# Performance work log

Measured on AMD Instinct MI355X. Metric: run time of the kernel, lower is better.

## Reference

```python
import jax, jax.numpy as jnp
import numpy as np

N = 50000          # nodes
E = 600000         # edges
D = 128            # g_dim = h1_dim = h2_dim
R = 8              # 2 * n_speakers**2, n_speakers=2
B = 10             # num_bases


def setup_inputs() -> dict:
    key = jax.random.key(0)
    ks = jax.random.split(key, 10)
    s = 1.0 / np.sqrt(D)
    return {
        "node_features": jax.random.normal(ks[0], (N, D), jnp.float32),
        "edge_index": jax.random.randint(ks[1], (2, E), 0, N, jnp.int64),
        "edge_type": jax.random.randint(ks[2], (E,), 0, R, jnp.int64),
        # RGCNConv params (basis decomposition)
        "basis": jax.random.normal(ks[3], (B, D, D), jnp.float32) * s,
        "comp": jax.random.normal(ks[4], (R, B), jnp.float32) * (1.0 / np.sqrt(B)),
        "root": jax.random.normal(ks[5], (D, D), jnp.float32) * s,
        "bias1": jnp.zeros((D,), jnp.float32),
        # GraphConv params
        "w_rel": jax.random.normal(ks[6], (D, D), jnp.float32) * s,
        "b_rel": jnp.zeros((D,), jnp.float32),
        "w_root": jax.random.normal(ks[7], (D, D), jnp.float32) * s,
    }


def reference(node_features, edge_index, edge_type, basis, comp, root, bias1, w_rel, b_rel, w_root):
    x = node_features
    n = x.shape[0]
    r = comp.shape[0]
    src, dst = edge_index[0], edge_index[1]

    # ---- RGCNConv (basis decomposition, per-relation mean aggregation) ----
    # project through bases once: [N, B, D]
    xb = jnp.einsum('ni,bio->nbo', x, basis)
    # per-edge message: combine bases with relation coefficients  [E, D]
    msg = jnp.einsum('eb,ebo->eo', comp[edge_type], xb[src])
    # per-(dst, relation) mean normalization
    seg = dst * r + edge_type                       # [E]
    cnt = jax.ops.segment_sum(jnp.ones((msg.shape[0],), x.dtype), seg, num_segments=n * r)
    norm = 1.0 / jnp.maximum(cnt[seg], 1.0)         # [E]
    agg = jax.ops.segment_sum(msg * norm[:, None], dst, num_segments=n)  # [N, D]
    h1 = agg + x @ root + bias1

    # ---- GraphConv (add aggregation of neighbors + root transform) ----
    nbr = jax.ops.segment_sum(h1[src], dst, num_segments=n)  # [N, D]
    out = nbr @ w_rel.T + b_rel + h1 @ w_root.T
    return out
```

## Files before the change

kernel.cpp:

```cpp
#include <hip/hip_runtime.h>
#include <stdint.h>

#define N_NODES 50000
#define E_EDGES 600000
#define D 128
#define R_REL 8
#define B_BASES 10
#define RN (R_REL * N_NODES)

typedef __attribute__((ext_vector_type(8))) short bf16x8;
typedef __attribute__((ext_vector_type(4))) float f32x4;

__device__ __forceinline__ short f2b(float f) {
    uint32_t u = __float_as_uint(f);
    u += 0x7fff + ((u >> 16) & 1);
    return (short)(u >> 16);
}
__device__ __forceinline__ float b2f(uint16_t u) {
    return __uint_as_float((uint32_t)u << 16);
}

__global__ __launch_bounds__(256) void k_front(const float* __restrict__ x,
                                               unsigned short* __restrict__ xb,
                                               const int* __restrict__ dst,
                                               const int* __restrict__ et,
                                               int* __restrict__ cntr,
                                               const float* __restrict__ basis,
                                               const float* __restrict__ comp,
                                               const float* __restrict__ root,
                                               const float* __restrict__ wrel,
                                               const float* __restrict__ wroot,
                                               short* __restrict__ wt,
                                               short* __restrict__ wrel_b,
                                               short* __restrict__ wroot_b) {
    const int XB_N = N_NODES * D / 8;
    int tid = blockIdx.x * 256 + threadIdx.x;
    if (tid < XB_N) {
        const float4* s = (const float4*)x + (size_t)tid * 2;
        float4 v0 = s[0], v1 = s[1];
        union { uint4 u; unsigned short h[8]; } pk;
        pk.h[0] = (unsigned short)f2b(v0.x); pk.h[1] = (unsigned short)f2b(v0.y);
        pk.h[2] = (unsigned short)f2b(v0.z); pk.h[3] = (unsigned short)f2b(v0.w);
        pk.h[4] = (unsigned short)f2b(v1.x); pk.h[5] = (unsigned short)f2b(v1.y);
        pk.h[6] = (unsigned short)f2b(v1.z); pk.h[7] = (unsigned short)f2b(v1.w);
        ((uint4*)xb)[tid] = pk.u;
    } else if (tid < XB_N + E_EDGES) {
        int e = tid - XB_N;
        atomicAdd(&cntr[dst[e] * R_REL + et[e]], 1);
    } else {
        int t2 = tid - XB_N - E_EDGES;
        if (t2 < 9 * D * D) {
            int s = t2 >> 14;
            int rem = t2 & 16383;
            int j = rem >> 7, i = rem & 127;
            float v;
            if (s < 8) {
                v = 0.f;
#pragma unroll
                for (int b = 0; b < B_BASES; b++)
                    v += comp[s * B_BASES + b] * basis[b * D * D + i * D + j];
            } else {
                v = root[i * D + j];
            }
            wt[t2] = f2b(v);
        } else {
            int t3 = t2 - 9 * D * D;
            if (t3 < D * D) {
                wrel_b[t3]  = f2b(wrel[t3]);
                wroot_b[t3] = f2b(wroot[t3]);
            }
        }
    }
}

__device__ __forceinline__ int wave_scan_incl(int v) {
    int lane = threadIdx.x & 63;
#pragma unroll
    for (int off = 1; off < 64; off <<= 1) {
        int n = __shfl_up(v, off, 64);
        if (lane >= off) v += n;
    }
    return v;
}

__global__ __launch_bounds__(1024) void k_scan_a(const int* __restrict__ in,
                                                 int* __restrict__ out,
                                                 int* __restrict__ bsum, int n) {
    __shared__ int wsum[16];
    int t = threadIdx.x, lane = t & 63, wid = t >> 6;
    int g = blockIdx.x * 1024 + t;
    int v = (g < n) ? in[g] : 0;
    int isc = wave_scan_incl(v);
    if (lane == 63) wsum[wid] = isc;
    __syncthreads();
    if (wid == 0) {
        int wv = (lane < 16) ? wsum[lane] : 0;
        int wsc = wave_scan_incl(wv);
        if (lane < 16) wsum[lane] = wsc - wv;
    }
    __syncthreads();
    if (g < n) out[g] = wsum[wid] + isc - v;
    if (t == 1023 && bsum) bsum[blockIdx.x] = wsum[15] + isc;
}

__global__ __launch_bounds__(1024) void k_scan_c(int* __restrict__ out,
                                                 const int* __restrict__ bsum, int n) {
    int g = blockIdx.x * 1024 + threadIdx.x;
    if (g < n) out[g] += bsum[blockIdx.x];
}

__global__ __launch_bounds__(256) void k_bucket(const int* __restrict__ src,
                                                const int* __restrict__ dst,
                                                const int* __restrict__ et,
                                                int* __restrict__ seg_off,
                                                int* __restrict__ es1) {
    int e = blockIdx.x * 256 + threadIdx.x;
    if (e >= E_EDGES) return;
    int key = dst[e] * R_REL + et[e];
    int pos = atomicAdd(&seg_off[key], 1);
    es1[pos] = src[e];
}

__global__ __launch_bounds__(256) void k_aggmean(const unsigned short* __restrict__ xb,
                                                 const int* __restrict__ es1,
                                                 const int* __restrict__ seg_off,
                                                 unsigned short* __restrict__ mx) {
    int t = threadIdx.x;
    int sw = t >> 4, l = t & 15;
    int k = blockIdx.x * 16 + sw;
    if (k >= RN) return;
    int start = (k == 0) ? 0 : seg_off[k - 1];
    int end = seg_off[k];
    float ax[8];
#pragma unroll
    for (int q = 0; q < 8; q++) ax[q] = 0.f;
    size_t loff = (size_t)l * 8;
    int pos = start;
    for (; pos + 2 <= end; pos += 2) {
        int s0 = es1[pos], s1 = es1[pos + 1];
        uint4 v0 = *(const uint4*)(xb + (size_t)s0 * D + loff);
        uint4 v1 = *(const uint4*)(xb + (size_t)s1 * D + loff);
        const uint32_t* w0 = (const uint32_t*)&v0;
        const uint32_t* w1 = (const uint32_t*)&v1;
#pragma unroll
        for (int q = 0; q < 4; q++) {
            ax[q * 2]     += b2f((uint16_t)w0[q]) + b2f((uint16_t)w1[q]);
            ax[q * 2 + 1] += b2f((uint16_t)(w0[q] >> 16)) + b2f((uint16_t)(w1[q] >> 16));
        }
    }
    if (pos < end) {
        int s0 = es1[pos];
        uint4 v0 = *(const uint4*)(xb + (size_t)s0 * D + loff);
        const uint32_t* w0 = (const uint32_t*)&v0;
#pragma unroll
        for (int q = 0; q < 4; q++) {
            ax[q * 2]     += b2f((uint16_t)w0[q]);
            ax[q * 2 + 1] += b2f((uint16_t)(w0[q] >> 16));
        }
    }
    float nm = (end > start) ? 1.f / (float)(end - start) : 0.f;
    union { uint4 u; unsigned short h[8]; } pk;
#pragma unroll
    for (int q = 0; q < 8; q++) pk.h[q] = (unsigned short)f2b(ax[q] * nm);
    *(uint4*)(mx + (size_t)k * D + loff) = pk.u;
}

__global__ __launch_bounds__(256) void k_h1_gemm(const unsigned short* __restrict__ mx,
                                                 const unsigned short* __restrict__ xb,
                                                 const short* __restrict__ wt,
                                                 const float* __restrict__ bias1,
                                                 unsigned short* __restrict__ h1b) {
    __shared__ short xs[64 * 128];
    __shared__ short ws[128 * 128];
    int base = blockIdx.x * 64;
    int t = threadIdx.x;
    int wave = t >> 6, lane = t & 63, quad = lane >> 4, l16 = lane & 15;
    f32x4 acc[8];
#pragma unroll
    for (int jt = 0; jt < 8; jt++) acc[jt] = (f32x4){0.f, 0.f, 0.f, 0.f};

    for (int s = 0; s < 9; s++) {
        __syncthreads();
        const uint4* wsrc = (const uint4*)(wt + (size_t)s * D * D);
        for (int idx = t; idx < 2048; idx += 256) {
            int j = idx >> 4, c = idx & 15;
            *(uint4*)&ws[j * 128 + ((c ^ (j & 15)) << 3)] = wsrc[idx];
        }
        for (int idx = t; idx < 1024; idx += 256) {
            int row = idx >> 4, c = idx & 15;
            int node = base + row;
            uint4 v = make_uint4(0, 0, 0, 0);
            if (node < N_NODES) {
                if (s < 8) v = ((const uint4*)(mx + ((size_t)node * 8 + s) * D))[c];
                else       v = ((const uint4*)(xb + (size_t)node * D))[c];
            }
            *(uint4*)&xs[row * 128 + ((c ^ (row & 15)) << 3)] = v;
        }
        __syncthreads();
#pragma unroll
        for (int kc = 0; kc < 4; kc++) {
            int c0 = kc * 4 + quad;
            bf16x8 a = *(const bf16x8*)&xs[(wave * 16 + l16) * 128 + ((c0 ^ l16) << 3)];
#pragma unroll
            for (int jt = 0; jt < 8; jt++) {
                bf16x8 b = *(const bf16x8*)&ws[(jt * 16 + l16) * 128 + ((c0 ^ l16) << 3)];
                acc[jt] = __builtin_amdgcn_mfma_f32_16x16x32_bf16(a, b, acc[jt], 0, 0, 0);
            }
        }
    }

#pragma unroll
    for (int reg = 0; reg < 4; reg++) {
        int node = base + wave * 16 + quad * 4 + reg;
        if (node >= N_NODES) continue;
#pragma unroll
        for (int jt = 0; jt < 8; jt++) {
            int col = jt * 16 + l16;
            float v = acc[jt][reg] + bias1[col];
            h1b[(size_t)node * D + col] = (unsigned short)f2b(v);
        }
    }
}

__global__ __launch_bounds__(256) void k_agg_nbr(const unsigned short* __restrict__ h1b,
                                                 const int* __restrict__ es1,
                                                 const int* __restrict__ seg_off,
                                                 unsigned short* __restrict__ nbr) {
    int t = threadIdx.x;
    int wave = t >> 6, lane = t & 63, sub = lane >> 4, l = lane & 15;
    int d = blockIdx.x * 16 + wave * 4 + sub;
    if (d >= N_NODES) return;
    int start = (d == 0) ? 0 : seg_off[d * R_REL - 1];
    int end = seg_off[d * R_REL + 7];
    float acc[8];
#pragma unroll
    for (int j = 0; j < 8; j++) acc[j] = 0.f;
    size_t loff = (size_t)l * 8;

    int pos = start;
    for (; pos + 4 <= end; pos += 4) {
        int i0 = es1[pos], i1 = es1[pos + 1], i2 = es1[pos + 2], i3 = es1[pos + 3];
        uint4 v0 = *(const uint4*)(h1b + (size_t)i0 * D + loff);
        uint4 v1 = *(const uint4*)(h1b + (size_t)i1 * D + loff);
        uint4 v2 = *(const uint4*)(h1b + (size_t)i2 * D + loff);
        uint4 v3 = *(const uint4*)(h1b + (size_t)i3 * D + loff);
        const uint32_t* w0 = (const uint32_t*)&v0;
        const uint32_t* w1 = (const uint32_t*)&v1;
        const uint32_t* w2 = (const uint32_t*)&v2;
        const uint32_t* w3 = (const uint32_t*)&v3;
#pragma unroll
        for (int q = 0; q < 4; q++) {
            acc[q * 2]     += b2f((uint16_t)w0[q]) + b2f((uint16_t)w1[q]) +
                              b2f((uint16_t)w2[q]) + b2f((uint16_t)w3[q]);
            acc[q * 2 + 1] += b2f((uint16_t)(w0[q] >> 16)) + b2f((uint16_t)(w1[q] >> 16)) +
                              b2f((uint16_t)(w2[q] >> 16)) + b2f((uint16_t)(w3[q] >> 16));
        }
    }
    for (; pos < end; pos++) {
        int i0 = es1[pos];
        uint4 v0 = *(const uint4*)(h1b + (size_t)i0 * D + loff);
        const uint32_t* w0 = (const uint32_t*)&v0;
#pragma unroll
        for (int q = 0; q < 4; q++) {
            acc[q * 2]     += b2f((uint16_t)w0[q]);
            acc[q * 2 + 1] += b2f((uint16_t)(w0[q] >> 16));
        }
    }

    union { uint4 u; unsigned short h[8]; } pk;
#pragma unroll
    for (int j = 0; j < 8; j++) pk.h[j] = (unsigned short)f2b(acc[j]);
    *(uint4*)(nbr + (size_t)d * D + loff) = pk.u;
}

__global__ __launch_bounds__(256) void k_out2(const unsigned short* __restrict__ h1b,
                                              const unsigned short* __restrict__ nbr,
                                              const short* __restrict__ wroot_b,
                                              const short* __restrict__ wrel_b,
                                              const float* __restrict__ brel,
                                              float* __restrict__ out) {
    __shared__ short xs1[64 * 128];
    __shared__ short xs2[64 * 128];
    __shared__ short ws1[128 * 128];
    __shared__ short ws2[128 * 128];
    int base = blockIdx.x * 64;
    int t = threadIdx.x;
    const uint4* w1 = (const uint4*)wroot_b;
    const uint4* w2 = (const uint4*)wrel_b;
    for (int idx = t; idx < 2048; idx += 256) {
        int j = idx >> 4, c = idx & 15;
        int sw = j * 128 + ((c ^ (j & 15)) << 3);
        *(uint4*)&ws1[sw] = w1[idx];
        *(uint4*)&ws2[sw] = w2[idx];
    }
    for (int idx = t; idx < 1024; idx += 256) {
        int row = idx >> 4, c = idx & 15;
        int node = base + row;
        uint4 v1 = make_uint4(0, 0, 0, 0), v2 = make_uint4(0, 0, 0, 0);
        if (node < N_NODES) {
            v1 = ((const uint4*)(h1b + (size_t)node * D))[c];
            v2 = ((const uint4*)(nbr + (size_t)node * D))[c];
        }
        int sw = row * 128 + ((c ^ (row & 15)) << 3);
        *(uint4*)&xs1[sw] = v1;
        *(uint4*)&xs2[sw] = v2;
    }
    __syncthreads();

    int wave = t >> 6, lane = t & 63, quad = lane >> 4, l16 = lane & 15;
    f32x4 acc[8];
#pragma unroll
    for (int jt = 0; jt < 8; jt++) acc[jt] = (f32x4){0.f, 0.f, 0.f, 0.f};
#pragma unroll
    for (int kc = 0; kc < 4; kc++) {
        int c0 = kc * 4 + quad;
        int arow = (wave * 16 + l16) * 128 + ((c0 ^ l16) << 3);
        bf16x8 a1 = *(const bf16x8*)&xs1[arow];
        bf16x8 a2 = *(const bf16x8*)&xs2[arow];
#pragma unroll
        for (int jt = 0; jt < 8; jt++) {
            int brow = (jt * 16 + l16) * 128 + ((c0 ^ l16) << 3);
            bf16x8 b1 = *(const bf16x8*)&ws1[brow];
            bf16x8 b2 = *(const bf16x8*)&ws2[brow];
            acc[jt] = __builtin_amdgcn_mfma_f32_16x16x32_bf16(a1, b1, acc[jt], 0, 0, 0);
            acc[jt] = __builtin_amdgcn_mfma_f32_16x16x32_bf16(a2, b2, acc[jt], 0, 0, 0);
        }
    }
#pragma unroll
    for (int reg = 0; reg < 4; reg++) {
        int node = base + wave * 16 + quad * 4 + reg;
        if (node >= N_NODES) continue;
#pragma unroll
        for (int jt = 0; jt < 8; jt++) {
            int col = jt * 16 + l16;
            out[(size_t)node * D + col] = acc[jt][reg] + brel[col];
        }
    }
}

extern "C" void kernel_launch(void* const* d_in, const int* in_sizes, int n_in,
                              void* d_out, int out_size, void* d_ws, size_t ws_size,
                              hipStream_t stream) {
    const float* x     = (const float*)d_in[0];
    const int*   ei    = (const int*)d_in[1];
    const int*   et    = (const int*)d_in[2];
    const float* basis = (const float*)d_in[3];
    const float* comp  = (const float*)d_in[4];
    const float* root  = (const float*)d_in[5];
    const float* bias1 = (const float*)d_in[6];
    const float* wrel  = (const float*)d_in[7];
    const float* brel  = (const float*)d_in[8];
    const float* wroot = (const float*)d_in[9];
    float* out = (float*)d_out;
    const int* src = ei;
    const int* dst = ei + E_EDGES;

    char* p = (char*)d_ws;
    auto alloc = [&](size_t bytes) { char* q = p; p += (bytes + 255) & ~(size_t)255; return q; };
    short* wt      = (short*)alloc((size_t)9 * D * D * sizeof(short));
    short* wrel_b  = (short*)alloc(D * D * sizeof(short));
    short* wroot_b = (short*)alloc(D * D * sizeof(short));
    int*   cntr    = (int*)alloc((size_t)RN * sizeof(int));
    int*   seg_off = (int*)alloc((size_t)RN * sizeof(int));
    int*   es1     = (int*)alloc((size_t)(E_EDGES + 16) * sizeof(int));
    int*   bsum    = (int*)alloc(1024 * sizeof(int));
    unsigned short* xb  = (unsigned short*)alloc((size_t)N_NODES * D * sizeof(unsigned short));
    unsigned short* mx  = (unsigned short*)alloc((size_t)RN * D * sizeof(unsigned short));
    unsigned short* h1b = (unsigned short*)alloc((size_t)N_NODES * D * sizeof(unsigned short));
    unsigned short* nbr = xb;

    hipMemsetAsync(cntr, 0, (size_t)RN * sizeof(int), stream);

    const int XB_N = N_NODES * D / 8;
    int nfront = (XB_N + E_EDGES + 9 * D * D + D * D + 255) / 256;
    k_front<<<nfront, 256, 0, stream>>>(x, xb, dst, et, cntr,
                                        basis, comp, root, wrel, wroot,
                                        wt, wrel_b, wroot_b);

    int nscan = (RN + 1023) / 1024;
    k_scan_a<<<nscan, 1024, 0, stream>>>(cntr, seg_off, bsum, RN);
    k_scan_a<<<1, 1024, 0, stream>>>(bsum, bsum, nullptr, nscan);
    k_scan_c<<<nscan, 1024, 0, stream>>>(seg_off, bsum, RN);

    k_bucket<<<(E_EDGES + 255) / 256, 256, 0, stream>>>(src, dst, et, seg_off, es1);

    k_aggmean<<<RN / 16, 256, 0, stream>>>(xb, es1, seg_off, mx);

    int nb = (N_NODES + 63) / 64;
    int na = (N_NODES + 15) / 16;
    k_h1_gemm<<<nb, 256, 0, stream>>>(mx, xb, wt, bias1, h1b);
    k_agg_nbr<<<na, 256, 0, stream>>>(h1b, es1, seg_off, nbr);
    k_out2<<<nb, 256, 0, stream>>>(h1b, nbr, wroot_b, wrel_b, brel, out);
}
```

Measured before the change: 311.6 us.

## Load GEMM operands directly from global memory instead of staging through LDS

```diff
diff --git a/kernel.cpp b/kernel.cpp
--- a/kernel.cpp
+++ b/kernel.cpp
@@ -170,40 +170,27 @@
                                                  const short* __restrict__ wt,
                                                  const float* __restrict__ bias1,
                                                  unsigned short* __restrict__ h1b) {
-    __shared__ short xs[64 * 128];
-    __shared__ short ws[128 * 128];
-    int base = blockIdx.x * 64;
     int t = threadIdx.x;
     int wave = t >> 6, lane = t & 63, quad = lane >> 4, l16 = lane & 15;
+    int arow_idx = blockIdx.x * 64 + wave * 16 + l16;
+    bool valid = arow_idx < N_NODES;
+    int nodeC = valid ? arow_idx : N_NODES - 1;
     f32x4 acc[8];
 #pragma unroll
     for (int jt = 0; jt < 8; jt++) acc[jt] = (f32x4){0.f, 0.f, 0.f, 0.f};
 
     for (int s = 0; s < 9; s++) {
-        __syncthreads();
-        const uint4* wsrc = (const uint4*)(wt + (size_t)s * D * D);
-        for (int idx = t; idx < 2048; idx += 256) {
-            int j = idx >> 4, c = idx & 15;
-            *(uint4*)&ws[j * 128 + ((c ^ (j & 15)) << 3)] = wsrc[idx];
-        }
-        for (int idx = t; idx < 1024; idx += 256) {
-            int row = idx >> 4, c = idx & 15;
-            int node = base + row;
-            uint4 v = make_uint4(0, 0, 0, 0);
-            if (node < N_NODES) {
-                if (s < 8) v = ((const uint4*)(mx + ((size_t)node * 8 + s) * D))[c];
-                else       v = ((const uint4*)(xb + (size_t)node * D))[c];
-            }
-            *(uint4*)&xs[row * 128 + ((c ^ (row & 15)) << 3)] = v;
-        }
-        __syncthreads();
+        const unsigned short* arow = (s < 8) ? mx + ((size_t)nodeC * 8 + s) * D
+                                             : xb + (size_t)nodeC * D;
+        const short* wbase = wt + (size_t)s * D * D;
 #pragma unroll
         for (int kc = 0; kc < 4; kc++) {
             int c0 = kc * 4 + quad;
-            bf16x8 a = *(const bf16x8*)&xs[(wave * 16 + l16) * 128 + ((c0 ^ l16) << 3)];
+            bf16x8 a = (bf16x8){0, 0, 0, 0, 0, 0, 0, 0};
+            if (valid) a = *(const bf16x8*)(arow + c0 * 8);
 #pragma unroll
             for (int jt = 0; jt < 8; jt++) {
-                bf16x8 b = *(const bf16x8*)&ws[(jt * 16 + l16) * 128 + ((c0 ^ l16) << 3)];
+                bf16x8 b = *(const bf16x8*)(wbase + (jt * 16 + l16) * D + c0 * 8);
                 acc[jt] = __builtin_amdgcn_mfma_f32_16x16x32_bf16(a, b, acc[jt], 0, 0, 0);
             }
         }
@@ -211,7 +198,7 @@
 
 #pragma unroll
     for (int reg = 0; reg < 4; reg++) {
-        int node = base + wave * 16 + quad * 4 + reg;
+        int node = blockIdx.x * 64 + wave * 16 + quad * 4 + reg;
         if (node >= N_NODES) continue;
 #pragma unroll
         for (int jt = 0; jt < 8; jt++) {
@@ -279,56 +266,35 @@
                                               const short* __restrict__ wrel_b,
                                               const float* __restrict__ brel,
                                               float* __restrict__ out) {
-    __shared__ short xs1[64 * 128];
-    __shared__ short xs2[64 * 128];
-    __shared__ short ws1[128 * 128];
-    __shared__ short ws2[128 * 128];
-    int base = blockIdx.x * 64;
     int t = threadIdx.x;
-    const uint4* w1 = (const uint4*)wroot_b;
-    const uint4* w2 = (const uint4*)wrel_b;
-    for (int idx = t; idx < 2048; idx += 256) {
-        int j = idx >> 4, c = idx & 15;
-        int sw = j * 128 + ((c ^ (j & 15)) << 3);
-        *(uint4*)&ws1[sw] = w1[idx];
-        *(uint4*)&ws2[sw] = w2[idx];
-    }
-    for (int idx = t; idx < 1024; idx += 256) {
-        int row = idx >> 4, c = idx & 15;
-        int node = base + row;
-        uint4 v1 = make_uint4(0, 0, 0, 0), v2 = make_uint4(0, 0, 0, 0);
-        if (node < N_NODES) {
-            v1 = ((const uint4*)(h1b + (size_t)node * D))[c];
-            v2 = ((const uint4*)(nbr + (size_t)node * D))[c];
-        }
-        int sw = row * 128 + ((c ^ (row & 15)) << 3);
-        *(uint4*)&xs1[sw] = v1;
-        *(uint4*)&xs2[sw] = v2;
-    }
-    __syncthreads();
-
     int wave = t >> 6, lane = t & 63, quad = lane >> 4, l16 = lane & 15;
+    int arow_idx = blockIdx.x * 64 + wave * 16 + l16;
+    bool valid = arow_idx < N_NODES;
+    int nodeC = valid ? arow_idx : N_NODES - 1;
     f32x4 acc[8];
 #pragma unroll
     for (int jt = 0; jt < 8; jt++) acc[jt] = (f32x4){0.f, 0.f, 0.f, 0.f};
-#pragma unroll
-    for (int kc = 0; kc < 4; kc++) {
-        int c0 = kc * 4 + quad;
-        int arow = (wave * 16 + l16) * 128 + ((c0 ^ l16) << 3);
-        bf16x8 a1 = *(const bf16x8*)&xs1[arow];
-        bf16x8 a2 = *(const bf16x8*)&xs2[arow];
-#pragma unroll
-        for (int jt = 0; jt < 8; jt++) {
-            int brow = (jt * 16 + l16) * 128 + ((c0 ^ l16) << 3);
-            bf16x8 b1 = *(const bf16x8*)&ws1[brow];
-            bf16x8 b2 = *(const bf16x8*)&ws2[brow];
-            acc[jt] = __builtin_amdgcn_mfma_f32_16x16x32_bf16(a1, b1, acc[jt], 0, 0, 0);
-            acc[jt] = __builtin_amdgcn_mfma_f32_16x16x32_bf16(a2, b2, acc[jt], 0, 0, 0);
-        }
-    }
+
+#pragma unroll
+    for (int pass = 0; pass < 2; pass++) {
+        const unsigned short* arow = (pass == 0 ? h1b : nbr) + (size_t)nodeC * D;
+        const short* wbase = pass == 0 ? wroot_b : wrel_b;
+#pragma unroll
+        for (int kc = 0; kc < 4; kc++) {
+            int c0 = kc * 4 + quad;
+            bf16x8 a = (bf16x8){0, 0, 0, 0, 0, 0, 0, 0};
+            if (valid) a = *(const bf16x8*)(arow + c0 * 8);
+#pragma unroll
+            for (int jt = 0; jt < 8; jt++) {
+                bf16x8 b = *(const bf16x8*)(wbase + (jt * 16 + l16) * D + c0 * 8);
+                acc[jt] = __builtin_amdgcn_mfma_f32_16x16x32_bf16(a, b, acc[jt], 0, 0, 0);
+            }
+        }
+    }
+
 #pragma unroll
     for (int reg = 0; reg < 4; reg++) {
-        int node = base + wave * 16 + quad * 4 + reg;
+        int node = blockIdx.x * 64 + wave * 16 + quad * 4 + reg;
         if (node >= N_NODES) continue;
 #pragma unroll
         for (int jt = 0; jt < 8; jt++) {
```

Measured after the change: 404.8 us. +29.9%, slower.
